# Optimization experiments

Hardware: AMD Instinct MI355X
Metric: run time of the kernel (lower is better)

The kernel has to match this reference:

```python
import jax, jax.numpy as jnp
import numpy as np

B, T, C, H, HD = 2, 2048, 2048, 16, 128
RD = HD // 2          # rope_dim = 64 (32 complex pairs)
KVR, QR = 512, 1024   # kv_lora_rank, q_lora_rank


def setup_inputs() -> dict:
    key = jax.random.key(0)
    ks = jax.random.split(key, 10)
    s = 0.02
    x = jax.random.normal(ks[0], (B, T, C), jnp.float32)
    w_dq  = jax.random.normal(ks[1], (C, QR),     jnp.float32) * s
    w_uq  = jax.random.normal(ks[2], (QR, H * HD), jnp.float32) * s
    w_dkv = jax.random.normal(ks[3], (C, KVR),    jnp.float32) * s
    w_uk  = jax.random.normal(ks[4], (KVR, H * HD), jnp.float32) * s
    w_uv  = jax.random.normal(ks[5], (KVR, H * HD), jnp.float32) * s
    w_qr  = jax.random.normal(ks[6], (QR, H * RD), jnp.float32) * s
    w_kr  = jax.random.normal(ks[7], (C, H * RD), jnp.float32) * s
    w_o   = jax.random.normal(ks[8], (H * HD, C), jnp.float32) * s
    # rotary frequencies for the rope_dim part (rope_dim//2 = 32 complex freqs)
    inv_freq = 1.0 / (10000.0 ** (jnp.arange(0, RD, 2, dtype=jnp.float32) / RD))
    ang = jnp.arange(T, dtype=jnp.float32)[:, None] * inv_freq[None, :]  # (T, 32)
    return {"x": x, "w_dq": w_dq, "w_uq": w_uq, "w_dkv": w_dkv, "w_uk": w_uk,
            "w_uv": w_uv, "w_qr": w_qr, "w_kr": w_kr, "w_o": w_o,
            "freqs_cos": jnp.cos(ang), "freqs_sin": jnp.sin(ang)}


def _apply_rope(t, cos, sin):
    # t: (B, T, H, rd); cos/sin: (T, rd//2). Complex rotation on adjacent pairs.
    tr, ti = t[..., 0::2], t[..., 1::2]
    c = cos[None, :, None, :]
    s = sin[None, :, None, :]
    out_r = tr * c - ti * s
    out_i = tr * s + ti * c
    return jnp.stack([out_r, out_i], axis=-1).reshape(t.shape)


def reference(x, w_dq, w_uq, w_dkv, w_uk, w_uv, w_qr, w_kr, w_o, freqs_cos, freqs_sin):
    b, t, _ = x.shape
    # low-rank KV path
    c_kv = x @ w_dkv                                   # (B,T,KVR)
    k_c = (c_kv @ w_uk).reshape(b, t, H, HD)
    v   = (c_kv @ w_uv).reshape(b, t, H, HD)
    # low-rank Q path
    c_q = x @ w_dq                                     # (B,T,QR)
    q_c = (c_q @ w_uq).reshape(b, t, H, HD)
    # decoupled rope parts
    q_r = (c_q @ w_qr).reshape(b, t, H, RD)
    k_r = (x @ w_kr).reshape(b, t, H, RD)
    q_r = _apply_rope(q_r, freqs_cos, freqs_sin)
    k_r = _apply_rope(k_r, freqs_cos, freqs_sin)
    # concat content + rope -> head dim D = HD + RD
    q = jnp.concatenate([q_c, q_r], axis=-1).transpose(0, 2, 1, 3)  # (B,H,T,D)
    k = jnp.concatenate([k_c, k_r], axis=-1).transpose(0, 2, 1, 3)
    v = v.transpose(0, 2, 1, 3)                                     # (B,H,T,HD)
    d = q.shape[-1]
    scores = jnp.einsum('bhqd,bhkd->bhqk', q, k) / jnp.sqrt(jnp.float32(d))
    causal = jnp.tril(jnp.ones((t, t), dtype=bool))
    scores = jnp.where(causal[None, None], scores, jnp.float32(-1e30))
    att = jax.nn.softmax(scores, axis=-1)
    out = jnp.einsum('bhqk,bhkd->bhqd', att, v)        # (B,H,T,HD)
    out = out.transpose(0, 2, 1, 3).reshape(b, t, H * HD)
    return out @ w_o
```

## Files before the change

### kernel.cpp

```cpp
#include <hip/hip_runtime.h>

typedef unsigned short ushort_t;
typedef __attribute__((ext_vector_type(8))) short bs8;
typedef __attribute__((ext_vector_type(4))) float f32x4;
typedef __attribute__((ext_vector_type(4))) unsigned short u16x4;

#define DEV __device__ __forceinline__

DEV unsigned short f2bf(float f){
  unsigned u = __float_as_uint(f);
  u += 0x7fffu + ((u >> 16) & 1u);
  return (unsigned short)(u >> 16);
}
DEV float bf2f(unsigned short h){ return __uint_as_float(((unsigned)h) << 16); }

DEV unsigned cvt_pk_bf16(float lo, float hi){
  unsigned r;
  asm volatile("v_cvt_pk_bf16_f32 %0, %1, %2" : "=v"(r) : "v"(lo), "v"(hi));
  return r;
}

DEV void gl2lds16(const void* g, void* l){
  __builtin_amdgcn_global_load_lds((const __attribute__((address_space(1))) void*)g,
                                   (__attribute__((address_space(3))) void*)l, 16, 0, 0);
}

DEV void st_out(ushort_t* C, size_t i, float v){ C[i] = f2bf(v); }
DEV void st_out(float*    C, size_t i, float v){ C[i] = v; }

__global__ __launch_bounds__(256) void prep_all(
    const float* __restrict__ x, ushort_t* __restrict__ xb,
    const float* __restrict__ s0, const float* __restrict__ s1,
    const float* __restrict__ s2, const float* __restrict__ s3,
    const float* __restrict__ s4, const float* __restrict__ s5,
    const float* __restrict__ s6, const float* __restrict__ s7,
    ushort_t* __restrict__ d0, ushort_t* __restrict__ d1,
    ushort_t* __restrict__ d2, ushort_t* __restrict__ d3,
    ushort_t* __restrict__ d4, ushort_t* __restrict__ d5,
    ushort_t* __restrict__ d6, ushort_t* __restrict__ d7){
  const int bid = blockIdx.x;
  if (bid >= 14336){
    size_t i = ((size_t)(bid - 14336) * 256 + threadIdx.x) * 4;
    float4 v = *(const float4*)(x + i);
    u16x4 o;
    o[0] = f2bf(v.x); o[1] = f2bf(v.y); o[2] = f2bf(v.z); o[3] = f2bf(v.w);
    *(u16x4*)(xb + i) = o;
    return;
  }
  __shared__ float tile[32][33];
  const float* src; ushort_t* dst; int K, N, loc;
  if      (bid <  2048){ src=s0; dst=d0; K=2048; N=1024; loc=bid; }
  else if (bid <  3072){ src=s1; dst=d1; K=2048; N=512;  loc=bid-2048; }
  else if (bid <  5120){ src=s2; dst=d2; K=2048; N=1024; loc=bid-3072; }
  else if (bid <  7168){ src=s3; dst=d3; K=1024; N=2048; loc=bid-5120; }
  else if (bid <  8192){ src=s4; dst=d4; K=1024; N=1024; loc=bid-7168; }
  else if (bid <  9216){ src=s5; dst=d5; K=512;  N=2048; loc=bid-8192; }
  else if (bid < 10240){ src=s6; dst=d6; K=512;  N=2048; loc=bid-9216; }
  else                 { src=s7; dst=d7; K=2048; N=2048; loc=bid-10240; }
  const int nx = N >> 5;
  const int n0 = (loc % nx) << 5, k0 = (loc / nx) << 5;
  const int tx = threadIdx.x & 31, ty = threadIdx.x >> 5;
  for (int r = ty; r < 32; r += 8)
    tile[r][tx] = src[(size_t)(k0 + r) * N + n0 + tx];
  __syncthreads();
  for (int r = ty; r < 32; r += 8)
    dst[(size_t)(n0 + r) * K + k0 + tx] = f2bf(tile[tx][r]);
}

DEV void gemm_core(const ushort_t* __restrict__ A, int lda,
                   const ushort_t* __restrict__ BT, int K,
                   int m0, int n0, ushort_t* lds, f32x4 (&acc)[8][4]){
  const int tid = threadIdx.x, lane = tid & 63, wid = tid >> 6;
  const int l15 = lane & 15, lhi = lane >> 4;
  const int wr = wid >> 2, wc = wid & 3;

  const int trow = tid >> 3;
  const int tcsrc = (tid & 7) ^ (trow & 7);
  const ushort_t* gA[2][2];
  const ushort_t* gB[2][2];
#pragma unroll
  for (int h = 0; h < 2; ++h)
#pragma unroll
    for (int i = 0; i < 2; ++i){
      gA[h][i] = A  + (size_t)(m0 + h * 128 + i * 64 + trow) * lda + tcsrc * 8;
      gB[h][i] = BT + (size_t)(n0 + h * 128 + i * 64 + trow) * K   + tcsrc * 8;
    }

  auto STAGE_A = [&](int buf, int h, int kt){
    gl2lds16(gA[h][0] + (size_t)kt * 64, lds + buf * 32768 + h * 8192 + tid * 8);
    gl2lds16(gA[h][1] + (size_t)kt * 64, lds + buf * 32768 + h * 8192 + 4096 + tid * 8);
  };
  auto STAGE_B = [&](int buf, int h, int kt){
    gl2lds16(gB[h][0] + (size_t)kt * 64, lds + buf * 32768 + 16384 + h * 8192 + tid * 8);
    gl2lds16(gB[h][1] + (size_t)kt * 64, lds + buf * 32768 + 16384 + h * 8192 + 4096 + tid * 8);
  };

  const int ck0 = ((lhi) ^ (l15 & 7)) << 3;
  const int ck1 = ((4 + lhi) ^ (l15 & 7)) << 3;

  bs8 aF[4][2], bLo[2][2], bHi[2][2];

  auto RDA = [&](int buf, int mq){
#pragma unroll
    for (int m = 0; m < 4; ++m){
      const ushort_t* r = lds + buf * 32768 + wr * 8192 + ((mq + m) * 16 + l15) * 64;
      aF[m][0] = *(const bs8*)(r + ck0);
      aF[m][1] = *(const bs8*)(r + ck1);
    }
  };
  auto RDB = [&](int buf, int nq, bs8 (&br)[2][2]){
#pragma unroll
    for (int n = 0; n < 2; ++n){
      const ushort_t* r = lds + buf * 32768 + 16384 + (wc >> 1) * 8192 +
                          ((wc & 1) * 64 + (nq + n) * 16 + l15) * 64;
      br[n][0] = *(const bs8*)(r + ck0);
      br[n][1] = *(const bs8*)(r + ck1);
    }
  };
  auto MMA = [&](int mq, int nq, bs8 (&br)[2][2]){
    __builtin_amdgcn_s_setprio(1);
#pragma unroll
    for (int m = 0; m < 4; ++m)
#pragma unroll
      for (int n = 0; n < 2; ++n){
        acc[mq + m][nq + n] = __builtin_amdgcn_mfma_f32_16x16x32_bf16(aF[m][0], br[n][0], acc[mq + m][nq + n], 0, 0, 0);
        acc[mq + m][nq + n] = __builtin_amdgcn_mfma_f32_16x16x32_bf16(aF[m][1], br[n][1], acc[mq + m][nq + n], 0, 0, 0);
      }
    __builtin_amdgcn_s_setprio(0);
  };

#define BAR() __builtin_amdgcn_s_barrier()
#define LGK() asm volatile("s_waitcnt lgkmcnt(0)" ::: "memory")
#define VMC4() asm volatile("s_waitcnt vmcnt(4)" ::: "memory")

  const int nkt = K >> 6;
  const int nIter = K >> 7;

  STAGE_A(0, 0, 0); STAGE_A(0, 1, 0); STAGE_B(0, 0, 0); STAGE_B(0, 1, 0);
  STAGE_B(1, 0, 1); STAGE_B(1, 1, 1);
  VMC4();
  BAR();

  for (int it = 0; it < nIter; ++it){
    const int kt1 = 2 * it + 1;
    int kt2 = 2 * it + 2; if (kt2 > nkt - 1) kt2 = nkt - 1;
    int kt3 = 2 * it + 3; if (kt3 > nkt - 1) kt3 = nkt - 1;
    RDA(0, 0); RDB(0, 0, bLo);
    STAGE_A(1, 0, kt1);
    BAR(); LGK(); MMA(0, 0, bLo); BAR();
    RDB(0, 2, bHi);
    STAGE_A(1, 1, kt1);
    BAR(); LGK(); MMA(0, 2, bHi); BAR();
    RDA(0, 4);
    STAGE_B(0, 0, kt2);
    BAR(); LGK(); MMA(4, 0, bLo); BAR();
    STAGE_B(0, 1, kt2);
    BAR(); LGK(); MMA(4, 2, bHi);
    VMC4(); BAR();
    RDA(1, 0); RDB(1, 0, bLo);
    STAGE_A(0, 0, kt2);
    BAR(); LGK(); MMA(0, 0, bLo); BAR();
    RDB(1, 2, bHi);
    STAGE_A(0, 1, kt2);
    BAR(); LGK(); MMA(0, 2, bHi); BAR();
    RDA(1, 4);
    STAGE_B(1, 0, kt3);
    BAR(); LGK(); MMA(4, 0, bLo); BAR();
    STAGE_B(1, 1, kt3);
    BAR(); LGK(); MMA(4, 2, bHi);
    VMC4(); BAR();
  }
#undef BAR
#undef LGK
#undef VMC4
}

template<int EPI, typename OT>
DEV void gemm_epi(f32x4 (&acc)[8][4], OT* __restrict__ C, int N, int m0, int n0,
                  ushort_t* __restrict__ aux,
                  const float* __restrict__ fcp, const float* __restrict__ fsp){
  const int tid = threadIdx.x, lane = tid & 63, wid = tid >> 6;
  const int l15 = lane & 15, lhi = lane >> 4;
  const int wr = wid >> 2, wc = wid & 3;
  const float SC = (EPI == 2) ? (0.07216878364870323f * 1.4426950408889634f) : 1.0f;
  const int RBASE = (EPI == 1) ? 1536 : 2048;
#pragma unroll
  for (int m = 0; m < 8; ++m){
    const int r = m0 + wr * 128 + m * 16 + lhi * 4;
#pragma unroll
    for (int n = 0; n < 4; ++n){
      const int c = n0 + wc * 64 + n * 16 + l15;
      if (EPI == 0){
#pragma unroll
        for (int j = 0; j < 4; ++j)
          st_out(C, (size_t)(r + j) * N + c, acc[m][n][j]);
      } else if ((EPI == 1 && c < 1536)){
#pragma unroll
        for (int j = 0; j < 4; ++j)
          C[(size_t)(r + j) * 1536 + c] = (OT)f2bf(acc[m][n][j]);
      } else if (EPI == 2 && c < 2048){
        int hh = c >> 7, d = c & 127;
#pragma unroll
        for (int j = 0; j < 4; ++j){
          int rr = r + j, bb = rr >> 11, tt = rr & 2047;
          aux[((size_t)(bb * 16 + hh) * 2048 + tt) * 192 + d] = f2bf(acc[m][n][j] * SC);
        }
      } else if (EPI == 3 && c < 2048){
        int hh = c >> 7, d = c & 127;
#pragma unroll
        for (int j = 0; j < 4; ++j){
          int rr = r + j, bb = rr >> 11, tt = rr & 2047;
          aux[((size_t)(bb * 16 + hh) * 2048 + tt) * 192 + d] = f2bf(acc[m][n][j]);
        }
      } else if (EPI == 3){
        int cv = c - 2048;
        int hh = cv >> 7, d = cv & 127;
        int bb = r >> 11, tt = r & 2047;
        u16x4 o;
#pragma unroll
        for (int j = 0; j < 4; ++j) o[j] = f2bf(acc[m][n][j]);
        *(u16x4*)((ushort_t*)C + ((size_t)(bb * 16 + hh) * 128 + d) * 2048 + tt) = o;
      } else {
        int cr = c - RBASE;
        int hh = cr >> 6, dr = cr & 63, ii = dr >> 1;
#pragma unroll
        for (int j = 0; j < 4; ++j){
          int rr = r + j, bb = rr >> 11, tt = rr & 2047;
          float v = acc[m][n][j] * SC;
          float pv = __shfl_xor(v, 1);
          float co = fcp[tt * 32 + ii], si = fsp[tt * 32 + ii];
          float o = (l15 & 1) ? fmaf(pv, si, v * co) : fmaf(-pv, si, v * co);
          aux[((size_t)(bb * 16 + hh) * 2048 + tt) * 192 + 128 + dr] = f2bf(o);
        }
      }
    }
  }
}

template<int EPI, typename OT>
__global__ __launch_bounds__(512, 2) void gemm256(const ushort_t* __restrict__ A, int lda,
                                                  const ushort_t* __restrict__ BT,
                                                  OT* __restrict__ C,
                                                  int M, int N, int K,
                                                  ushort_t* __restrict__ aux,
                                                  const float* __restrict__ fcp,
                                                  const float* __restrict__ fsp){
  __shared__ __align__(16) ushort_t lds[65536];
  const int nbx = M >> 8;
  const int nwg = gridDim.x;
  const int orig = blockIdx.x;
  const int wg = (orig & 7) * (nwg >> 3) + (orig >> 3);
  const int m0 = (wg % nbx) << 8;
  const int n0 = (wg / nbx) << 8;
  f32x4 acc[8][4] = {};
  gemm_core(A, lda, BT, K, m0, n0, lds, acc);
  gemm_epi<EPI, OT>(acc, C, N, m0, n0, aux, fcp, fsp);
}

__global__ __launch_bounds__(512, 2) void gemm23(const ushort_t* __restrict__ A2,
                                                 const ushort_t* __restrict__ BT2,
                                                 const ushort_t* __restrict__ A3,
                                                 const ushort_t* __restrict__ BT3,
                                                 ushort_t* __restrict__ vT,
                                                 ushort_t* __restrict__ Qa,
                                                 ushort_t* __restrict__ Ka,
                                                 const float* __restrict__ fcp,
                                                 const float* __restrict__ fsp){
  __shared__ __align__(16) ushort_t lds[65536];
  const int nwg = gridDim.x;
  const int orig = blockIdx.x;
  const int wg = (orig & 7) * (nwg >> 3) + (orig >> 3);
  f32x4 acc[8][4] = {};
  if (wg < 192){
    const int m0 = (wg % 16) << 8, n0 = (wg / 16) << 8;
    gemm_core(A2, 1536, BT2, 1024, m0, n0, lds, acc);
    gemm_epi<2, ushort_t>(acc, nullptr, 3072, m0, n0, Qa, fcp, fsp);
  } else {
    const int g = wg - 192;
    const int m0 = (g % 16) << 8, n0 = (g / 16) << 8;
    gemm_core(A3, 1536, BT3, 512, m0, n0, lds, acc);
    gemm_epi<3, ushort_t>(acc, vT, 4096, m0, n0, Ka, fcp, fsp);
  }
}

__global__ __launch_bounds__(512, 1) void gemm4_128(const ushort_t* __restrict__ A, int lda,
                                                    const ushort_t* __restrict__ BT,
                                                    float* __restrict__ C,
                                                    int M, int N, int K){
  __shared__ __align__(16) ushort_t lds[49152];
  const int tid = threadIdx.x, lane = tid & 63, wid = tid >> 6;
  const int l15 = lane & 15, lhi = lane >> 4;
  const int wr = wid >> 1, wc = wid & 1;

  const int nbx = M >> 8;
  const int nwg = gridDim.x;
  const int orig = blockIdx.x;
  const int wg = (orig & 7) * (nwg >> 3) + (orig >> 3);
  const int m0 = (wg % nbx) << 8;
  const int n0 = (wg / nbx) << 7;

  const int trow = tid >> 3;
  const int tcsrc = (tid & 7) ^ (trow & 7);
  const ushort_t* gA[2][2];
  const ushort_t* gB[2];
#pragma unroll
  for (int h = 0; h < 2; ++h)
#pragma unroll
    for (int i = 0; i < 2; ++i)
      gA[h][i] = A + (size_t)(m0 + h * 128 + i * 64 + trow) * lda + tcsrc * 8;
#pragma unroll
  for (int i = 0; i < 2; ++i)
    gB[i] = BT + (size_t)(n0 + i * 64 + trow) * K + tcsrc * 8;

  auto STAGE_A = [&](int buf, int h, int kt){
    gl2lds16(gA[h][0] + (size_t)kt * 64, lds + buf * 24576 + h * 8192 + tid * 8);
    gl2lds16(gA[h][1] + (size_t)kt * 64, lds + buf * 24576 + h * 8192 + 4096 + tid * 8);
  };
  auto STAGE_B = [&](int buf, int kt){
    gl2lds16(gB[0] + (size_t)kt * 64, lds + buf * 24576 + 16384 + tid * 8);
    gl2lds16(gB[1] + (size_t)kt * 64, lds + buf * 24576 + 16384 + 4096 + tid * 8);
  };

  const int ck0 = ((lhi) ^ (l15 & 7)) << 3;
  const int ck1 = ((4 + lhi) ^ (l15 & 7)) << 3;

  f32x4 acc[4][4] = {};
  bs8 aF[2][2], bLo[2][2], bHi[2][2];

  auto RDA = [&](int buf, int mq){
#pragma unroll
    for (int m = 0; m < 2; ++m){
      const int rowin = (wr & 1) * 64 + (mq + m) * 16 + l15;
      const ushort_t* r = lds + buf * 24576 + (wr >> 1) * 8192 + rowin * 64;
      aF[m][0] = *(const bs8*)(r + ck0);
      aF[m][1] = *(const bs8*)(r + ck1);
    }
  };
  auto RDB = [&](int buf, int nq, bs8 (&br)[2][2]){
#pragma unroll
    for (int n = 0; n < 2; ++n){
      const int row = wc * 64 + (nq + n) * 16 + l15;
      const ushort_t* r = lds + buf * 24576 + 16384 + row * 64;
      br[n][0] = *(const bs8*)(r + ck0);
      br[n][1] = *(const bs8*)(r + ck1);
    }
  };
  auto MMA = [&](int mq, int nq, bs8 (&br)[2][2]){
    __builtin_amdgcn_s_setprio(1);
#pragma unroll
    for (int m = 0; m < 2; ++m)
#pragma unroll
      for (int n = 0; n < 2; ++n){
        acc[mq + m][nq + n] = __builtin_amdgcn_mfma_f32_16x16x32_bf16(aF[m][0], br[n][0], acc[mq + m][nq + n], 0, 0, 0);
        acc[mq + m][nq + n] = __builtin_amdgcn_mfma_f32_16x16x32_bf16(aF[m][1], br[n][1], acc[mq + m][nq + n], 0, 0, 0);
      }
    __builtin_amdgcn_s_setprio(0);
  };

#define BAR() __builtin_amdgcn_s_barrier()
#define LGK() asm volatile("s_waitcnt lgkmcnt(0)" ::: "memory")
#define VMC2() asm volatile("s_waitcnt vmcnt(2)" ::: "memory")

  const int nkt = K >> 6;
  const int nIter = K >> 7;

  STAGE_A(0, 0, 0); STAGE_A(0, 1, 0); STAGE_B(0, 0);
  STAGE_B(1, 1);
  VMC2();
  BAR();

  for (int it = 0; it < nIter; ++it){
    const int kt1 = 2 * it + 1;
    int kt2 = 2 * it + 2; if (kt2 > nkt - 1) kt2 = nkt - 1;
    int kt3 = 2 * it + 3; if (kt3 > nkt - 1) kt3 = nkt - 1;
    RDA(0, 0); RDB(0, 0, bLo);
    STAGE_A(1, 0, kt1);
    BAR(); LGK(); MMA(0, 0, bLo); BAR();
    RDB(0, 2, bHi);
    STAGE_A(1, 1, kt1);
    BAR(); LGK(); MMA(0, 2, bHi); BAR();
    RDA(0, 2);
    STAGE_B(0, kt2);
    BAR(); LGK(); MMA(2, 0, bLo); BAR();
    BAR(); LGK(); MMA(2, 2, bHi);
    VMC2(); BAR();
    RDA(1, 0); RDB(1, 0, bLo);
    STAGE_A(0, 0, kt2);
    BAR(); LGK(); MMA(0, 0, bLo); BAR();
    RDB(1, 2, bHi);
    STAGE_A(0, 1, kt2);
    BAR(); LGK(); MMA(0, 2, bHi); BAR();
    RDA(1, 2);
    STAGE_B(1, kt3);
    BAR(); LGK(); MMA(2, 0, bLo); BAR();
    BAR(); LGK(); MMA(2, 2, bHi);
    VMC2(); BAR();
  }
#undef BAR
#undef LGK
#undef VMC2

#pragma unroll
  for (int m = 0; m < 4; ++m){
    const int r = m0 + wr * 64 + m * 16 + lhi * 4;
#pragma unroll
    for (int n = 0; n < 4; ++n){
      const int c = n0 + wc * 64 + n * 16 + l15;
#pragma unroll
      for (int j = 0; j < 4; ++j)
        C[(size_t)(r + j) * N + c] = acc[m][n][j];
    }
  }
}

__global__ __launch_bounds__(512) void attn_kernel(const ushort_t* __restrict__ Qa,
                                                   const ushort_t* __restrict__ Ka,
                                                   const ushort_t* __restrict__ VT,
                                                   ushort_t* __restrict__ O){
  __shared__ __align__(16) ushort_t lds[40960];
  const int tid = threadIdx.x, lane = tid & 63, wid = tid >> 6;
  const int bh = blockIdx.x;
  const int y = blockIdx.y;
  const int qb = (y < 8) ? (15 - y) : (y - 8);
  const int b = bh >> 4, h = bh & 15;
  const int qm0 = qb << 7;
  const int nkt = 2 * qb + 2;
  const int l15 = lane & 15, lhi = lane >> 4;

  const ushort_t* Kbh = Ka + (size_t)bh * 2048 * 192;
  const ushort_t* Vbh = VT + (size_t)bh * 128 * 2048;

  const ushort_t* ksrc[3];
#pragma unroll
  for (int i = 0; i < 3; ++i){
    int c = i * 512 + tid;
    int row = c / 24, col = c % 24;
    int hk = (row & 3) | (((row >> 3) & 1) << 2);
    ksrc[i] = Kbh + (size_t)row * 192 + (col ^ hk) * 8;
  }
  const ushort_t* vsrc[2];
#pragma unroll
  for (int i = 0; i < 2; ++i){
    int c = i * 512 + tid;
    int d = c >> 3, col = c & 7;
    vsrc[i] = Vbh + (size_t)d * 2048 + (col ^ (d & 7)) * 8;
  }

  auto STAGE = [&](int kt, int buf){
#pragma unroll
    for (int i = 0; i < 3; ++i)
      gl2lds16(ksrc[i] + (size_t)kt * 12288, lds + buf * 12288 + (i * 512 + tid) * 8);
#pragma unroll
    for (int i = 0; i < 2; ++i)
      gl2lds16(vsrc[i] + kt * 64, lds + 24576 + buf * 8192 + (i * 512 + tid) * 8);
  };

  bs8 qf[6];
  {
    const size_t qrow = ((size_t)bh * 2048 + qm0 + wid * 16 + l15) * 192;
#pragma unroll
    for (int kc = 0; kc < 6; ++kc)
      qf[kc] = *(const bs8*)(Qa + qrow + kc * 32 + lhi * 8);
  }

  f32x4 acc[8] = {};
  float mrow = -1e30f, lrow = 0.f;

  const int mylast = 2 * qb + (wid >> 2);
  const int hkr = (l15 & 3) | (((l15 >> 2) & 1) << 2);

#define BARR() __builtin_amdgcn_s_barrier()
#define LGK0() asm volatile("s_waitcnt lgkmcnt(0)" ::: "memory")
#define VMC(n) asm volatile("s_waitcnt vmcnt(" #n ")" ::: "memory")

  STAGE(0, 0);
  STAGE(1, 1);
  VMC(5);
  BARR();

  for (int kt = 0; kt < nkt; ++kt){
    const int cur = kt & 1;
    const ushort_t* Kb = lds + cur * 12288;
    const ushort_t* Vb = lds + 24576 + cur * 8192;

    if (kt <= mylast){
      f32x4 s[4] = {};
      __builtin_amdgcn_s_setprio(1);
#pragma unroll
      for (int kc = 0; kc < 6; ++kc){
        bs8 kf4[4];
#pragma unroll
        for (int m = 0; m < 4; ++m){
          int row = ((m >> 1) << 5) + ((l15 >> 2) << 3) + ((m & 1) << 2) + (l15 & 3);
          kf4[m] = *(const bs8*)(Kb + row * 192 + (((kc * 4 + lhi) ^ hkr) << 3));
        }
#pragma unroll
        for (int m = 0; m < 4; ++m)
          s[m] = __builtin_amdgcn_mfma_f32_16x16x32_bf16(kf4[m], qf[kc], s[m], 0, 0, 0);
      }
      __builtin_amdgcn_s_setprio(0);

      const bool noMask = (kt * 64 + 63) <= (qm0 + wid * 16);
      const int qi = qm0 + wid * 16 + l15;
      if (!noMask){
#pragma unroll
        for (int m = 0; m < 4; ++m)
#pragma unroll
          for (int j = 0; j < 4; ++j){
            int ki = kt * 64 + ((m >> 1) << 5) + (lhi << 3) + ((m & 1) << 2) + j;
            if (ki > qi) s[m][j] = -3e38f;
          }
      }
      float r0 = fmaxf(fmaxf(s[0][0], s[0][1]), s[0][2]);
      float r1 = fmaxf(fmaxf(s[0][3], s[1][0]), s[1][1]);
      float r2 = fmaxf(fmaxf(s[1][2], s[1][3]), s[2][0]);
      float r3 = fmaxf(fmaxf(s[2][1], s[2][2]), s[2][3]);
      float r4 = fmaxf(fmaxf(s[3][0], s[3][1]), s[3][2]);
      float rmax = fmaxf(fmaxf(r0, r1), fmaxf(fmaxf(r2, r3), fmaxf(r4, s[3][3])));
      rmax = fmaxf(rmax, __shfl_xor(rmax, 16));
      rmax = fmaxf(rmax, __shfl_xor(rmax, 32));
      if (!__all(rmax <= mrow + 8.f)){
        float mnew = fmaxf(mrow, rmax);
        float osc = exp2f(mrow - mnew);
        lrow *= osc;
#pragma unroll
        for (int f = 0; f < 8; ++f) acc[f] *= osc;
        mrow = mnew;
      }
      float rsum = 0.f;
#pragma unroll
      for (int m = 0; m < 4; ++m)
#pragma unroll
        for (int j = 0; j < 4; ++j){
          float pv = exp2f(s[m][j] - mrow);
          s[m][j] = pv;
          rsum += pv;
        }
      rsum += __shfl_xor(rsum, 16);
      rsum += __shfl_xor(rsum, 32);
      lrow += rsum;

      bs8 pb[2];
#pragma unroll
      for (int kc2 = 0; kc2 < 2; ++kc2){
        union { bs8 v; unsigned u[4]; } pu;
#pragma unroll
        for (int half = 0; half < 2; ++half){
          const f32x4& sv = s[2 * kc2 + half];
          pu.u[2 * half]     = cvt_pk_bf16(sv[0], sv[1]);
          pu.u[2 * half + 1] = cvt_pk_bf16(sv[2], sv[3]);
        }
        pb[kc2] = pu.v;
      }

      __builtin_amdgcn_s_setprio(1);
#pragma unroll
      for (int kc2 = 0; kc2 < 2; ++kc2)
#pragma unroll
        for (int f = 0; f < 8; ++f){
          bs8 vf = *(const bs8*)(Vb + (f * 16 + l15) * 64 + (((kc2 * 4 + lhi) ^ (l15 & 7)) << 3));
          acc[f] = __builtin_amdgcn_mfma_f32_16x16x32_bf16(vf, pb[kc2], acc[f], 0, 0, 0);
        }
      __builtin_amdgcn_s_setprio(0);
    }

    LGK0();
    BARR();
    if (kt + 2 < nkt){
      STAGE(kt + 2, cur);
      VMC(5);
    } else {
      VMC(0);
    }
    BARR();
  }
#undef BARR
#undef LGK0
#undef VMC

  {
    float rl = 1.0f / lrow;
    int t = qm0 + wid * 16 + l15;
#pragma unroll
    for (int f = 0; f < 8; ++f){
      u16x4 o;
#pragma unroll
      for (int j = 0; j < 4; ++j) o[j] = f2bf(acc[f][j] * rl);
      *(u16x4*)(O + ((size_t)b * 2048 + t) * 2048 + h * 128 + f * 16 + lhi * 4) = o;
    }
  }
}

extern "C" void kernel_launch(void* const* d_in, const int* in_sizes, int n_in,
                              void* d_out, int out_size, void* d_ws, size_t ws_size,
                              hipStream_t stream){
  constexpr int Bc = 2, Tc = 2048, Cc = 2048, Hc = 16, HDc = 128, RDc = 64, KVRc = 512, QRc = 1024;
  constexpr int Mx = Bc * Tc;
  const float* x     = (const float*)d_in[0];
  const float* w_dq  = (const float*)d_in[1];
  const float* w_uq  = (const float*)d_in[2];
  const float* w_dkv = (const float*)d_in[3];
  const float* w_uk  = (const float*)d_in[4];
  const float* w_uv  = (const float*)d_in[5];
  const float* w_qr  = (const float*)d_in[6];
  const float* w_kr  = (const float*)d_in[7];
  const float* w_o   = (const float*)d_in[8];
  const float* fc    = (const float*)d_in[9];
  const float* fs    = (const float*)d_in[10];
  float* out = (float*)d_out;

  char* ws = (char*)d_ws;
  size_t off = 0;
  auto alloc = [&](size_t elems) -> ushort_t* {
    ushort_t* p = (ushort_t*)(ws + off);
    off += ((elems * 2) + 255) & ~(size_t)255;
    return p;
  };
  ushort_t* xb    = alloc((size_t)Mx * Cc);
  ushort_t* wdqT  = alloc((size_t)QRc * Cc);
  ushort_t* wdkvT = alloc((size_t)KVRc * Cc);
  ushort_t* wkrT  = alloc((size_t)(Hc * RDc) * Cc);
  ushort_t* wuqT  = alloc((size_t)(Hc * HDc) * QRc);
  ushort_t* wqrT  = alloc((size_t)(Hc * RDc) * QRc);
  ushort_t* wukT  = alloc((size_t)(Hc * HDc) * KVRc);
  ushort_t* wuvT  = alloc((size_t)(Hc * HDc) * KVRc);
  ushort_t* woT   = alloc((size_t)Cc * (Hc * HDc));
  ushort_t* comb1 = alloc((size_t)Mx * 1536);
  ushort_t* Qa    = alloc((size_t)Bc * Hc * Tc * 192);
  ushort_t* Ka    = alloc((size_t)Bc * Hc * Tc * 192);
  ushort_t* vT    = alloc((size_t)Bc * Hc * HDc * Tc);
  ushort_t* O     = xb;

  prep_all<<<dim3(14336 + 8192), 256, 0, stream>>>(x, xb,
      w_dq, w_dkv, w_kr, w_uq, w_qr, w_uk, w_uv, w_o,
      wdqT, wdkvT, wkrT, wuqT, wqrT, wukT, wuvT, woT);

  gemm256<1, ushort_t><<<dim3((Mx / 256) * (2560 / 256)), 512, 0, stream>>>(
      xb, Cc, wdqT, comb1, Mx, 2560, Cc, Ka, fc, fs);
  gemm23<<<dim3(448), 512, 0, stream>>>(comb1, wuqT, comb1 + QRc, wukT, vT, Qa, Ka, fc, fs);

  attn_kernel<<<dim3(Bc * Hc, 16), 512, 0, stream>>>(Qa, Ka, vT, O);

  gemm4_128<<<dim3(256), 512, 0, stream>>>(O, Hc * HDc, woT, out, Mx, Cc, Hc * HDc);
}
```

Baseline: 275.4 us.

## Replace 256x256 projection GEMMs with 256x128 tiles and simpler K-loop

The first-stage and second-stage projection GEMMs now use 256x128 output tiles with a K-step of 32 instead of 256x256 tiles with a K-step of 64. The main loop becomes a plain double-buffered loop, and LDS per block drops from 128 KB to 48 KB. Grid sizes double (320 and 896 blocks), which fills the CUs more evenly and allows more resident blocks. The cost is less data reuse per tile, more barriers per unit of K, and more redundant A-tile loads.

```diff
diff --git a/kernel.cpp b/kernel.cpp
--- a/kernel.cpp
+++ b/kernel.cpp
@@ -24,9 +24,6 @@
   __builtin_amdgcn_global_load_lds((const __attribute__((address_space(1))) void*)g,
                                    (__attribute__((address_space(3))) void*)l, 16, 0, 0);
 }
-
-DEV void st_out(ushort_t* C, size_t i, float v){ C[i] = f2bf(v); }
-DEV void st_out(float*    C, size_t i, float v){ C[i] = v; }
 
 __global__ __launch_bounds__(256) void prep_all(
     const float* __restrict__ x, ushort_t* __restrict__ xb,
@@ -67,118 +64,83 @@
     dst[(size_t)(n0 + r) * K + k0 + tx] = f2bf(tile[tx][r]);
 }
 
-DEV void gemm_core(const ushort_t* __restrict__ A, int lda,
-                   const ushort_t* __restrict__ BT, int K,
-                   int m0, int n0, ushort_t* lds, f32x4 (&acc)[8][4]){
+DEV void gemmS_core(const ushort_t* __restrict__ A, int lda,
+                    const ushort_t* __restrict__ BT, int K,
+                    int m0, int n0, ushort_t* lds, f32x4 (&acc)[8][2]){
   const int tid = threadIdx.x, lane = tid & 63, wid = tid >> 6;
   const int l15 = lane & 15, lhi = lane >> 4;
   const int wr = wid >> 2, wc = wid & 3;
 
-  const int trow = tid >> 3;
-  const int tcsrc = (tid & 7) ^ (trow & 7);
-  const ushort_t* gA[2][2];
-  const ushort_t* gB[2][2];
-#pragma unroll
-  for (int h = 0; h < 2; ++h)
-#pragma unroll
-    for (int i = 0; i < 2; ++i){
-      gA[h][i] = A  + (size_t)(m0 + h * 128 + i * 64 + trow) * lda + tcsrc * 8;
-      gB[h][i] = BT + (size_t)(n0 + h * 128 + i * 64 + trow) * K   + tcsrc * 8;
-    }
-
-  auto STAGE_A = [&](int buf, int h, int kt){
-    gl2lds16(gA[h][0] + (size_t)kt * 64, lds + buf * 32768 + h * 8192 + tid * 8);
-    gl2lds16(gA[h][1] + (size_t)kt * 64, lds + buf * 32768 + h * 8192 + 4096 + tid * 8);
-  };
-  auto STAGE_B = [&](int buf, int h, int kt){
-    gl2lds16(gB[h][0] + (size_t)kt * 64, lds + buf * 32768 + 16384 + h * 8192 + tid * 8);
-    gl2lds16(gB[h][1] + (size_t)kt * 64, lds + buf * 32768 + 16384 + h * 8192 + 4096 + tid * 8);
-  };
-
-  const int ck0 = ((lhi) ^ (l15 & 7)) << 3;
-  const int ck1 = ((4 + lhi) ^ (l15 & 7)) << 3;
-
-  bs8 aF[4][2], bLo[2][2], bHi[2][2];
-
-  auto RDA = [&](int buf, int mq){
-#pragma unroll
-    for (int m = 0; m < 4; ++m){
-      const ushort_t* r = lds + buf * 32768 + wr * 8192 + ((mq + m) * 16 + l15) * 64;
-      aF[m][0] = *(const bs8*)(r + ck0);
-      aF[m][1] = *(const bs8*)(r + ck1);
-    }
-  };
-  auto RDB = [&](int buf, int nq, bs8 (&br)[2][2]){
-#pragma unroll
-    for (int n = 0; n < 2; ++n){
-      const ushort_t* r = lds + buf * 32768 + 16384 + (wc >> 1) * 8192 +
-                          ((wc & 1) * 64 + (nq + n) * 16 + l15) * 64;
-      br[n][0] = *(const bs8*)(r + ck0);
-      br[n][1] = *(const bs8*)(r + ck1);
-    }
-  };
-  auto MMA = [&](int mq, int nq, bs8 (&br)[2][2]){
+  const ushort_t* ga[2];
+  int arow[2];
+#pragma unroll
+  for (int i = 0; i < 2; ++i){
+    int c = tid + i * 512;
+    int row = c >> 2, col = (c & 3) ^ (row & 3);
+    arow[i] = c;
+    ga[i] = A + (size_t)(m0 + row) * lda + col * 8;
+  }
+  const ushort_t* gb;
+  {
+    int row = tid >> 2, col = (tid & 3) ^ (row & 3);
+    gb = BT + (size_t)(n0 + row) * K + col * 8;
+  }
+
+  auto STAGE = [&](int kt, int buf){
+    gl2lds16(ga[0] + kt * 32, lds + buf * 8192 + arow[0] * 8);
+    gl2lds16(ga[1] + kt * 32, lds + buf * 8192 + arow[1] * 8);
+    gl2lds16(gb    + kt * 32, lds + 16384 + buf * 4096 + tid * 8);
+  };
+
+  const int ck = ((lhi ^ (l15 & 3)) << 3);
+  const int nkt = K >> 5;
+
+#define BARR() __builtin_amdgcn_s_barrier()
+#define LGK0() asm volatile("s_waitcnt lgkmcnt(0)" ::: "memory")
+#define VMC(n) asm volatile("s_waitcnt vmcnt(" #n ")" ::: "memory")
+
+  STAGE(0, 0);
+  STAGE(1, 1);
+  VMC(3);
+  BARR();
+
+  for (int kt = 0; kt < nkt; ++kt){
+    const int cur = kt & 1;
+    const ushort_t* Ab = lds + cur * 8192;
+    const ushort_t* Bb = lds + 16384 + cur * 4096;
+
+    bs8 bF[2];
+#pragma unroll
+    for (int n = 0; n < 2; ++n)
+      bF[n] = *(const bs8*)(Bb + (wc * 32 + n * 16 + l15) * 32 + ck);
     __builtin_amdgcn_s_setprio(1);
 #pragma unroll
-    for (int m = 0; m < 4; ++m)
-#pragma unroll
-      for (int n = 0; n < 2; ++n){
-        acc[mq + m][nq + n] = __builtin_amdgcn_mfma_f32_16x16x32_bf16(aF[m][0], br[n][0], acc[mq + m][nq + n], 0, 0, 0);
-        acc[mq + m][nq + n] = __builtin_amdgcn_mfma_f32_16x16x32_bf16(aF[m][1], br[n][1], acc[mq + m][nq + n], 0, 0, 0);
-      }
+    for (int m = 0; m < 8; ++m){
+      bs8 aF = *(const bs8*)(Ab + (wr * 128 + m * 16 + l15) * 32 + ck);
+      acc[m][0] = __builtin_amdgcn_mfma_f32_16x16x32_bf16(aF, bF[0], acc[m][0], 0, 0, 0);
+      acc[m][1] = __builtin_amdgcn_mfma_f32_16x16x32_bf16(aF, bF[1], acc[m][1], 0, 0, 0);
+    }
     __builtin_amdgcn_s_setprio(0);
-  };
-
-#define BAR() __builtin_amdgcn_s_barrier()
-#define LGK() asm volatile("s_waitcnt lgkmcnt(0)" ::: "memory")
-#define VMC4() asm volatile("s_waitcnt vmcnt(4)" ::: "memory")
-
-  const int nkt = K >> 6;
-  const int nIter = K >> 7;
-
-  STAGE_A(0, 0, 0); STAGE_A(0, 1, 0); STAGE_B(0, 0, 0); STAGE_B(0, 1, 0);
-  STAGE_B(1, 0, 1); STAGE_B(1, 1, 1);
-  VMC4();
-  BAR();
-
-  for (int it = 0; it < nIter; ++it){
-    const int kt1 = 2 * it + 1;
-    int kt2 = 2 * it + 2; if (kt2 > nkt - 1) kt2 = nkt - 1;
-    int kt3 = 2 * it + 3; if (kt3 > nkt - 1) kt3 = nkt - 1;
-    RDA(0, 0); RDB(0, 0, bLo);
-    STAGE_A(1, 0, kt1);
-    BAR(); LGK(); MMA(0, 0, bLo); BAR();
-    RDB(0, 2, bHi);
-    STAGE_A(1, 1, kt1);
-    BAR(); LGK(); MMA(0, 2, bHi); BAR();
-    RDA(0, 4);
-    STAGE_B(0, 0, kt2);
-    BAR(); LGK(); MMA(4, 0, bLo); BAR();
-    STAGE_B(0, 1, kt2);
-    BAR(); LGK(); MMA(4, 2, bHi);
-    VMC4(); BAR();
-    RDA(1, 0); RDB(1, 0, bLo);
-    STAGE_A(0, 0, kt2);
-    BAR(); LGK(); MMA(0, 0, bLo); BAR();
-    RDB(1, 2, bHi);
-    STAGE_A(0, 1, kt2);
-    BAR(); LGK(); MMA(0, 2, bHi); BAR();
-    RDA(1, 4);
-    STAGE_B(1, 0, kt3);
-    BAR(); LGK(); MMA(4, 0, bLo); BAR();
-    STAGE_B(1, 1, kt3);
-    BAR(); LGK(); MMA(4, 2, bHi);
-    VMC4(); BAR();
-  }
-#undef BAR
-#undef LGK
-#undef VMC4
+
+    LGK0();
+    BARR();
+    if (kt + 2 < nkt){
+      STAGE(kt + 2, cur);
+      VMC(3);
+    } else {
+      VMC(0);
+    }
+    BARR();
+  }
+#undef BARR
+#undef LGK0
+#undef VMC
 }
 
 template<int EPI, typename OT>
-DEV void gemm_epi(f32x4 (&acc)[8][4], OT* __restrict__ C, int N, int m0, int n0,
-                  ushort_t* __restrict__ aux,
-                  const float* __restrict__ fcp, const float* __restrict__ fsp){
+DEV void gemmS_epi(f32x4 (&acc)[8][2], OT* __restrict__ C, int m0, int n0,
+                   ushort_t* __restrict__ aux,
+                   const float* __restrict__ fcp, const float* __restrict__ fsp){
   const int tid = threadIdx.x, lane = tid & 63, wid = tid >> 6;
   const int l15 = lane & 15, lhi = lane >> 4;
   const int wr = wid >> 2, wc = wid & 3;
@@ -188,13 +150,9 @@
   for (int m = 0; m < 8; ++m){
     const int r = m0 + wr * 128 + m * 16 + lhi * 4;
 #pragma unroll
-    for (int n = 0; n < 4; ++n){
-      const int c = n0 + wc * 64 + n * 16 + l15;
-      if (EPI == 0){
-#pragma unroll
-        for (int j = 0; j < 4; ++j)
-          st_out(C, (size_t)(r + j) * N + c, acc[m][n][j]);
-      } else if ((EPI == 1 && c < 1536)){
+    for (int n = 0; n < 2; ++n){
+      const int c = n0 + wc * 32 + n * 16 + l15;
+      if (EPI == 1 && c < 1536){
 #pragma unroll
         for (int j = 0; j < 4; ++j)
           C[(size_t)(r + j) * 1536 + c] = (OT)f2bf(acc[m][n][j]);
@@ -237,49 +195,48 @@
   }
 }
 
-template<int EPI, typename OT>
-__global__ __launch_bounds__(512, 2) void gemm256(const ushort_t* __restrict__ A, int lda,
-                                                  const ushort_t* __restrict__ BT,
-                                                  OT* __restrict__ C,
-                                                  int M, int N, int K,
-                                                  ushort_t* __restrict__ aux,
-                                                  const float* __restrict__ fcp,
-                                                  const float* __restrict__ fsp){
-  __shared__ __align__(16) ushort_t lds[65536];
+__global__ __launch_bounds__(512, 2) void gemmS1(const ushort_t* __restrict__ A, int lda,
+                                                 const ushort_t* __restrict__ BT,
+                                                 ushort_t* __restrict__ C,
+                                                 int M, int K,
+                                                 ushort_t* __restrict__ aux,
+                                                 const float* __restrict__ fcp,
+                                                 const float* __restrict__ fsp){
+  __shared__ __align__(16) ushort_t lds[24576];
   const int nbx = M >> 8;
   const int nwg = gridDim.x;
   const int orig = blockIdx.x;
   const int wg = (orig & 7) * (nwg >> 3) + (orig >> 3);
   const int m0 = (wg % nbx) << 8;
-  const int n0 = (wg / nbx) << 8;
-  f32x4 acc[8][4] = {};
-  gemm_core(A, lda, BT, K, m0, n0, lds, acc);
-  gemm_epi<EPI, OT>(acc, C, N, m0, n0, aux, fcp, fsp);
-}
-
-__global__ __launch_bounds__(512, 2) void gemm23(const ushort_t* __restrict__ A2,
-                                                 const ushort_t* __restrict__ BT2,
-                                                 const ushort_t* __restrict__ A3,
-                                                 const ushort_t* __restrict__ BT3,
-                                                 ushort_t* __restrict__ vT,
-                                                 ushort_t* __restrict__ Qa,
-                                                 ushort_t* __restrict__ Ka,
-                                                 const float* __restrict__ fcp,
-                                                 const float* __restrict__ fsp){
-  __shared__ __align__(16) ushort_t lds[65536];
+  const int n0 = (wg / nbx) << 7;
+  f32x4 acc[8][2] = {};
+  gemmS_core(A, lda, BT, K, m0, n0, lds, acc);
+  gemmS_epi<1, ushort_t>(acc, C, m0, n0, aux, fcp, fsp);
+}
+
+__global__ __launch_bounds__(512, 2) void gemmS23(const ushort_t* __restrict__ A2,
+                                                  const ushort_t* __restrict__ BT2,
+                                                  const ushort_t* __restrict__ A3,
+                                                  const ushort_t* __restrict__ BT3,
+                                                  ushort_t* __restrict__ vT,
+                                                  ushort_t* __restrict__ Qa,
+                                                  ushort_t* __restrict__ Ka,
+                                                  const float* __restrict__ fcp,
+                                                  const float* __restrict__ fsp){
+  __shared__ __align__(16) ushort_t lds[24576];
   const int nwg = gridDim.x;
   const int orig = blockIdx.x;
   const int wg = (orig & 7) * (nwg >> 3) + (orig >> 3);
-  f32x4 acc[8][4] = {};
-  if (wg < 192){
-    const int m0 = (wg % 16) << 8, n0 = (wg / 16) << 8;
-    gemm_core(A2, 1536, BT2, 1024, m0, n0, lds, acc);
-    gemm_epi<2, ushort_t>(acc, nullptr, 3072, m0, n0, Qa, fcp, fsp);
+  f32x4 acc[8][2] = {};
+  if (wg < 384){
+    const int m0 = (wg % 16) << 8, n0 = (wg / 16) << 7;
+    gemmS_core(A2, 1536, BT2, 1024, m0, n0, lds, acc);
+    gemmS_epi<2, ushort_t>(acc, Qa, m0, n0, Qa, fcp, fsp);
   } else {
-    const int g = wg - 192;
-    const int m0 = (g % 16) << 8, n0 = (g / 16) << 8;
-    gemm_core(A3, 1536, BT3, 512, m0, n0, lds, acc);
-    gemm_epi<3, ushort_t>(acc, vT, 4096, m0, n0, Ka, fcp, fsp);
+    const int g = wg - 384;
+    const int m0 = (g % 16) << 8, n0 = (g / 16) << 7;
+    gemmS_core(A3, 1536, BT3, 512, m0, n0, lds, acc);
+    gemmS_epi<3, ushort_t>(acc, vT, m0, n0, Ka, fcp, fsp);
   }
 }
 
@@ -635,9 +592,8 @@
       w_dq, w_dkv, w_kr, w_uq, w_qr, w_uk, w_uv, w_o,
       wdqT, wdkvT, wkrT, wuqT, wqrT, wukT, wuvT, woT);
 
-  gemm256<1, ushort_t><<<dim3((Mx / 256) * (2560 / 256)), 512, 0, stream>>>(
-      xb, Cc, wdqT, comb1, Mx, 2560, Cc, Ka, fc, fs);
-  gemm23<<<dim3(448), 512, 0, stream>>>(comb1, wuqT, comb1 + QRc, wukT, vT, Qa, Ka, fc, fs);
+  gemmS1<<<dim3(320), 512, 0, stream>>>(xb, Cc, wdqT, comb1, Mx, Cc, Ka, fc, fs);
+  gemmS23<<<dim3(896), 512, 0, stream>>>(comb1, wuqT, comb1 + QRc, wukT, vT, Qa, Ka, fc, fs);
 
   attn_kernel<<<dim3(Bc * Hc, 16), 512, 0, stream>>>(Qa, Ka, vT, O);
 
```

Result: slower. 290.9 us (+5.6%).

## Overlap later weight transposes with first GEMM in a fused launch

Applied to the files above, without the earlier changes.

Splits the prep kernel so only x and the weights the first GEMM needs are converted up front. The transpose-to-bf16 of the remaining weights (w_uq, w_qr, w_uk, w_uv, w_o) moves into extra workgroups of the first GEMM launch, each doing two 32x32 tiles using the GEMM's LDS. The aim is to overlap that memory-bound conversion with the compute-bound GEMM instead of running it serially beforehand. The cost is a larger mixed-role grid, and the swizzled block mapping must still assign exactly the GEMM tiles and every transpose tile.

```diff
diff --git a/kernel.cpp b/kernel.cpp
--- a/kernel.cpp
+++ b/kernel.cpp
@@ -28,19 +28,15 @@
 DEV void st_out(ushort_t* C, size_t i, float v){ C[i] = f2bf(v); }
 DEV void st_out(float*    C, size_t i, float v){ C[i] = v; }
 
-__global__ __launch_bounds__(256) void prep_all(
+__global__ __launch_bounds__(256) void prep1(
     const float* __restrict__ x, ushort_t* __restrict__ xb,
     const float* __restrict__ s0, const float* __restrict__ s1,
-    const float* __restrict__ s2, const float* __restrict__ s3,
-    const float* __restrict__ s4, const float* __restrict__ s5,
-    const float* __restrict__ s6, const float* __restrict__ s7,
+    const float* __restrict__ s2,
     ushort_t* __restrict__ d0, ushort_t* __restrict__ d1,
-    ushort_t* __restrict__ d2, ushort_t* __restrict__ d3,
-    ushort_t* __restrict__ d4, ushort_t* __restrict__ d5,
-    ushort_t* __restrict__ d6, ushort_t* __restrict__ d7){
+    ushort_t* __restrict__ d2){
   const int bid = blockIdx.x;
-  if (bid >= 14336){
-    size_t i = ((size_t)(bid - 14336) * 256 + threadIdx.x) * 4;
+  if (bid < 8192){
+    size_t i = ((size_t)bid * 256 + threadIdx.x) * 4;
     float4 v = *(const float4*)(x + i);
     u16x4 o;
     o[0] = f2bf(v.x); o[1] = f2bf(v.y); o[2] = f2bf(v.z); o[3] = f2bf(v.w);
@@ -49,14 +45,9 @@
   }
   __shared__ float tile[32][33];
   const float* src; ushort_t* dst; int K, N, loc;
-  if      (bid <  2048){ src=s0; dst=d0; K=2048; N=1024; loc=bid; }
-  else if (bid <  3072){ src=s1; dst=d1; K=2048; N=512;  loc=bid-2048; }
-  else if (bid <  5120){ src=s2; dst=d2; K=2048; N=1024; loc=bid-3072; }
-  else if (bid <  7168){ src=s3; dst=d3; K=1024; N=2048; loc=bid-5120; }
-  else if (bid <  8192){ src=s4; dst=d4; K=1024; N=1024; loc=bid-7168; }
-  else if (bid <  9216){ src=s5; dst=d5; K=512;  N=2048; loc=bid-8192; }
-  else if (bid < 10240){ src=s6; dst=d6; K=512;  N=2048; loc=bid-9216; }
-  else                 { src=s7; dst=d7; K=2048; N=2048; loc=bid-10240; }
+  if      (bid < 10240){ src=s0; dst=d0; K=2048; N=1024; loc=bid-8192;  }
+  else if (bid < 11264){ src=s1; dst=d1; K=2048; N=512;  loc=bid-10240; }
+  else                 { src=s2; dst=d2; K=2048; N=1024; loc=bid-11264; }
   const int nx = N >> 5;
   const int n0 = (loc % nx) << 5, k0 = (loc / nx) << 5;
   const int tx = threadIdx.x & 31, ty = threadIdx.x >> 5;
@@ -237,24 +228,47 @@
   }
 }
 
-template<int EPI, typename OT>
-__global__ __launch_bounds__(512, 2) void gemm256(const ushort_t* __restrict__ A, int lda,
-                                                  const ushort_t* __restrict__ BT,
-                                                  OT* __restrict__ C,
-                                                  int M, int N, int K,
-                                                  ushort_t* __restrict__ aux,
-                                                  const float* __restrict__ fcp,
-                                                  const float* __restrict__ fsp){
+__global__ __launch_bounds__(512, 2) void gemm1f(const ushort_t* __restrict__ A, int lda,
+                                                 const ushort_t* __restrict__ BT,
+                                                 ushort_t* __restrict__ C, int K,
+                                                 ushort_t* __restrict__ aux,
+                                                 const float* __restrict__ fcp,
+                                                 const float* __restrict__ fsp,
+                                                 const float* __restrict__ t0s, ushort_t* __restrict__ t0d,
+                                                 const float* __restrict__ t1s, ushort_t* __restrict__ t1d,
+                                                 const float* __restrict__ t2s, ushort_t* __restrict__ t2d,
+                                                 const float* __restrict__ t3s, ushort_t* __restrict__ t3d,
+                                                 const float* __restrict__ t4s, ushort_t* __restrict__ t4d){
   __shared__ __align__(16) ushort_t lds[65536];
-  const int nbx = M >> 8;
   const int nwg = gridDim.x;
   const int orig = blockIdx.x;
   const int wg = (orig & 7) * (nwg >> 3) + (orig >> 3);
-  const int m0 = (wg % nbx) << 8;
-  const int n0 = (wg / nbx) << 8;
-  f32x4 acc[8][4] = {};
-  gemm_core(A, lda, BT, K, m0, n0, lds, acc);
-  gemm_epi<EPI, OT>(acc, C, N, m0, n0, aux, fcp, fsp);
+  if (wg < 160){
+    const int m0 = (wg % 16) << 8;
+    const int n0 = (wg / 16) << 8;
+    f32x4 acc[8][4] = {};
+    gemm_core(A, lda, BT, K, m0, n0, lds, acc);
+    gemm_epi<1, ushort_t>(acc, C, 2560, m0, n0, aux, fcp, fsp);
+    return;
+  }
+  const int tid = threadIdx.x;
+  const int tg = tid >> 8, tid2 = tid & 255;
+  const int tileid = 2 * (wg - 160) + tg;
+  const float* src; ushort_t* dst; int K2, N2, loc;
+  if      (tileid < 2048){ src=t0s; dst=t0d; K2=1024; N2=2048; loc=tileid; }
+  else if (tileid < 3072){ src=t1s; dst=t1d; K2=1024; N2=1024; loc=tileid-2048; }
+  else if (tileid < 4096){ src=t2s; dst=t2d; K2=512;  N2=2048; loc=tileid-3072; }
+  else if (tileid < 5120){ src=t3s; dst=t3d; K2=512;  N2=2048; loc=tileid-4096; }
+  else                   { src=t4s; dst=t4d; K2=2048; N2=2048; loc=tileid-5120; }
+  const int nx = N2 >> 5;
+  const int n0 = (loc % nx) << 5, k0 = (loc / nx) << 5;
+  float* tl = (float*)lds + tg * 1068;
+  const int tx = tid2 & 31, ty = tid2 >> 5;
+  for (int r = ty; r < 32; r += 8)
+    tl[r * 33 + tx] = src[(size_t)(k0 + r) * N2 + n0 + tx];
+  __syncthreads();
+  for (int r = ty; r < 32; r += 8)
+    dst[(size_t)(n0 + r) * K2 + k0 + tx] = f2bf(tl[tx * 33 + r]);
 }
 
 __global__ __launch_bounds__(512, 2) void gemm23(const ushort_t* __restrict__ A2,
@@ -631,12 +645,12 @@
   ushort_t* vT    = alloc((size_t)Bc * Hc * HDc * Tc);
   ushort_t* O     = xb;
 
-  prep_all<<<dim3(14336 + 8192), 256, 0, stream>>>(x, xb,
-      w_dq, w_dkv, w_kr, w_uq, w_qr, w_uk, w_uv, w_o,
-      wdqT, wdkvT, wkrT, wuqT, wqrT, wukT, wuvT, woT);
-
-  gemm256<1, ushort_t><<<dim3((Mx / 256) * (2560 / 256)), 512, 0, stream>>>(
-      xb, Cc, wdqT, comb1, Mx, 2560, Cc, Ka, fc, fs);
+  prep1<<<dim3(13312), 256, 0, stream>>>(x, xb, w_dq, w_dkv, w_kr, wdqT, wdkvT, wkrT);
+
+  gemm1f<<<dim3(4768), 512, 0, stream>>>(
+      xb, Cc, wdqT, comb1, Cc, Ka, fc, fs,
+      w_uq, wuqT, w_qr, wqrT, w_uk, wukT, w_uv, wuvT, w_o, woT);
+
   gemm23<<<dim3(448), 512, 0, stream>>>(comb1, wuqT, comb1 + QRc, wukT, vT, Qa, Ka, fc, fs);
 
   attn_kernel<<<dim3(Bc * Hc, 16), 512, 0, stream>>>(Qa, Ka, vT, O);
```

Result: slower. 493.5 us (+79.2%).
